# Kernel tuning notes

Measured on AMD Instinct MI355X. Metric: run time of the kernel, lower is better.

## Reference

```python
import jax, jax.numpy as jnp
import numpy as np

B, L = 16, 4096
D_IN, D_OUT, D_MODEL, N_LAYERS, N_STATE = 257, 257, 256, 4, 32  # 32 complex modes (= d_state 64 real)


def setup_inputs() -> dict:
    key = jax.random.key(0)
    ks = iter(jax.random.split(key, 24))
    nrm = lambda shape, s=0.02: jax.random.normal(next(ks), shape, jnp.float32) * s
    H, N = D_MODEL, N_STATE
    return {
        "x": jax.random.normal(next(ks), (B, L, D_IN, 2), jnp.float32),
        "enc_Wr": nrm((D_MODEL, D_IN)), "enc_Wi": nrm((D_MODEL, D_IN)),
        "enc_br": jnp.zeros((D_MODEL,), jnp.float32), "enc_bi": jnp.zeros((D_MODEL,), jnp.float32),
        # per layer (N_LAYERS) and per complex branch (2: real-branch S4D, imag-branch S4D)
        "s4_log_dt": jax.random.uniform(next(ks), (N_LAYERS, 2, H), jnp.float32,
                                        minval=float(np.log(0.001)), maxval=float(np.log(0.1))),
        "s4_log_A_real": jnp.broadcast_to(jnp.log(0.5 * jnp.ones((H, N), jnp.float32)), (N_LAYERS, 2, H, N)) + 0.0,
        "s4_A_imag": jnp.broadcast_to(jnp.pi * jnp.arange(N, dtype=jnp.float32), (N_LAYERS, 2, H, N)) + 0.0,
        "s4_C": jax.random.normal(next(ks), (N_LAYERS, 2, H, N, 2), jnp.float32) * (0.5 ** 0.5),
        "s4_D": jax.random.normal(next(ks), (N_LAYERS, 2, H), jnp.float32),
        "s4_Wout": nrm((N_LAYERS, 2, 2 * H, H)), "s4_bout": jnp.zeros((N_LAYERS, 2, 2 * H), jnp.float32),
        "ln_gamma": jnp.ones((N_LAYERS, 2, H), jnp.float32), "ln_beta": jnp.zeros((N_LAYERS, 2, H), jnp.float32),
        "dec_Wr": nrm((D_OUT, D_MODEL)), "dec_Wi": nrm((D_OUT, D_MODEL)),
        "dec_br": jnp.zeros((D_OUT,), jnp.float32), "dec_bi": jnp.zeros((D_OUT,), jnp.float32),
    }


def complex_linear(xr, xi, Wr, Wi, br, bi):
    yr = xr @ Wr.T - xi @ Wi.T + br
    yi = xr @ Wi.T + xi @ Wr.T + bi
    return yr, yi


def s4d_branch(u, log_dt, log_A_real, A_imag, C2, D, Wout, bout):
    """Standard S4D-minimal layer. u: (B, H, L) real."""
    Ln = u.shape[-1]
    dt = jnp.exp(log_dt)                            # (H,)
    A = -jnp.exp(log_A_real) + 1j * A_imag          # (H, N) complex
    C = C2[..., 0] + 1j * C2[..., 1]                # (H, N)
    dtA = A * dt[:, None]                           # (H, N)
    Cmod = C * (jnp.exp(dtA) - 1.0) / A
    vand = jnp.exp(dtA[..., None] * jnp.arange(Ln)) # (H, N, L)
    k = 2.0 * jnp.einsum('hn,hnl->hl', Cmod, vand).real  # (H, L)
    kf = jnp.fft.rfft(k, n=2 * Ln)
    uf = jnp.fft.rfft(u, n=2 * Ln)
    y = jnp.fft.irfft(uf * kf[None], n=2 * Ln)[..., :Ln]  # causal conv
    y = y + u * D[:, None]
    y = jax.nn.gelu(y, approximate=False)
    y = jnp.einsum('oh,bhl->bol', Wout, y) + bout[None, :, None]  # 1x1 conv to 2H
    a, g = jnp.split(y, 2, axis=1)                  # GLU over channel dim
    return a * jax.nn.sigmoid(g)


def layer_norm(x, gamma, beta):
    # x: (B, L, H), normalize over H (biased variance, like torch LayerNorm)
    mu = x.mean(-1, keepdims=True)
    var = x.var(-1, keepdims=True)
    return (x - mu) / jnp.sqrt(var + 1e-5) * gamma + beta


def reference(x, enc_Wr, enc_Wi, enc_br, enc_bi,
              s4_log_dt, s4_log_A_real, s4_A_imag, s4_C, s4_D, s4_Wout, s4_bout,
              ln_gamma, ln_beta, dec_Wr, dec_Wi, dec_br, dec_bi):
    xr, xi = complex_linear(x[..., 0], x[..., 1], enc_Wr, enc_Wi, enc_br, enc_bi)  # (B, L, H)
    xr = xr.swapaxes(-1, -2)  # (B, H, L)
    xi = xi.swapaxes(-1, -2)
    for l in range(N_LAYERS):
        sr = lambda u: s4d_branch(u, s4_log_dt[l, 0], s4_log_A_real[l, 0], s4_A_imag[l, 0],
                                  s4_C[l, 0], s4_D[l, 0], s4_Wout[l, 0], s4_bout[l, 0])
        si = lambda u: s4d_branch(u, s4_log_dt[l, 1], s4_log_A_real[l, 1], s4_A_imag[l, 1],
                                  s4_C[l, 1], s4_D[l, 1], s4_Wout[l, 1], s4_bout[l, 1])
        zr = sr(xr) - si(xi)
        zi = sr(xi) + si(xr)
        xr = xr + zr  # residual (dropout = identity)
        xi = xi + zi
        # post-norm over d_model (separate LN for real/imag parts)
        xr = layer_norm(xr.swapaxes(-1, -2), ln_gamma[l, 0], ln_beta[l, 0]).swapaxes(-1, -2)
        xi = layer_norm(xi.swapaxes(-1, -2), ln_gamma[l, 1], ln_beta[l, 1]).swapaxes(-1, -2)
    xr = xr.swapaxes(-1, -2)  # (B, L, H)
    xi = xi.swapaxes(-1, -2)
    yr, yi = complex_linear(xr, xi, dec_Wr, dec_Wi, dec_br, dec_bi)  # (B, L, D_OUT)
    return jnp.stack([yr, yi], axis=-1)
```

## Files before the change

### kernel.cpp

```cpp
#include <hip/hip_runtime.h>

typedef unsigned short ushort_t;
typedef unsigned int uint_t;
typedef __attribute__((ext_vector_type(8))) short short8;
typedef __attribute__((ext_vector_type(4))) float f32x4;

#define B_    16
#define L_    4096
#define H_    256
#define N_    32
#define DIN_  257
#define DOUT_ 257
#define NL_   4
#define Q_    128
#define NC_   32
#define BL_   (B_*L_)
#define NH_   (N_*H_)
#define PLANE_ 16777216
#define SSZ_  4194304
#define EPK_  520

__device__ __forceinline__ float bfu(ushort_t u) {
    union { uint_t i; float f; } v; v.i = ((uint_t)u) << 16; return v.f;
}
__device__ __forceinline__ ushort_t f2bf(float f) {
    union { float f; uint_t i; } v; v.f = f;
    uint_t x = v.i;
    return (ushort_t)((x + 0x7FFFu + ((x >> 16) & 1u)) >> 16);
}
__device__ __forceinline__ uint2 pack4(float a, float b, float c, float d) {
    uint2 r;
    r.x = (uint_t)f2bf(a) | ((uint_t)f2bf(b) << 16);
    r.y = (uint_t)f2bf(c) | ((uint_t)f2bf(d) << 16);
    return r;
}
__device__ __forceinline__ float ldi(const void* p, size_t i, int f32) {
    return f32 ? ((const float*)p)[i] : bfu(((const ushort_t*)p)[i]);
}

__device__ __forceinline__ void gl16(const ushort_t* g, ushort_t* l) {
    __builtin_amdgcn_global_load_lds(
        (const __attribute__((address_space(1))) uint_t*)g,
        (__attribute__((address_space(3))) uint_t*)l, 16, 0, 0);
}

__device__ __forceinline__ uint4 ld8bf(const void* W, size_t eoff, int f32) {
    uint4 r;
    if (f32) {
        const float* p = (const float*)W + eoff;
        float4 a = *(const float4*)p;
        float4 b = *(const float4*)(p + 4);
        r.x = (uint_t)f2bf(a.x) | ((uint_t)f2bf(a.y) << 16);
        r.y = (uint_t)f2bf(a.z) | ((uint_t)f2bf(a.w) << 16);
        r.z = (uint_t)f2bf(b.x) | ((uint_t)f2bf(b.y) << 16);
        r.w = (uint_t)f2bf(b.z) | ((uint_t)f2bf(b.w) << 16);
    } else {
        r = *(const uint4*)((const ushort_t*)W + eoff);
    }
    return r;
}

__device__ __forceinline__ uint4 ld8r(const void* x, size_t eoff, int f32) {
    uint4 r;
    if (f32) {
        const float* p = (const float*)x + eoff;
        float2 a = *(const float2*)p;
        float2 b = *(const float2*)(p + 2);
        float2 c = *(const float2*)(p + 4);
        float2 d = *(const float2*)(p + 6);
        r.x = (uint_t)f2bf(a.x) | ((uint_t)f2bf(a.y) << 16);
        r.y = (uint_t)f2bf(b.x) | ((uint_t)f2bf(b.y) << 16);
        r.z = (uint_t)f2bf(c.x) | ((uint_t)f2bf(c.y) << 16);
        r.w = (uint_t)f2bf(d.x) | ((uint_t)f2bf(d.y) << 16);
    } else {
        const uint_t* q = (const uint_t*)((const ushort_t*)x + eoff);
        r.x = q[0]; r.y = q[1]; r.z = q[2]; r.w = q[3];
    }
    return r;
}

__device__ __forceinline__ short8 negbf(short8 v) {
    short8 r;
#pragma unroll
    for (int i = 0; i < 8; ++i) r[i] = (short)(v[i] ^ (short)0x8000);
    return r;
}

#define MFMA16(a, b, c) __builtin_amdgcn_mfma_f32_16x16x32_bf16((a), (b), (c), 0, 0, 0)

__global__ void probe_kernel(const void* __restrict__ x, int* __restrict__ flag) {
    __shared__ int cnt;
    if (threadIdx.x == 0) cnt = 0;
    __syncthreads();
    uint_t w = ((const uint_t*)x)[threadIdx.x];
    float f = bfu((ushort_t)(w & 0xFFFF));
    float a = fabsf(f);
    if (a > 1e-5f && a < 100.f) atomicAdd(&cnt, 1);
    __syncthreads();
    if (threadIdx.x == 0) *flag = (cnt > 128) ? 0 : 1;
}

__global__ __launch_bounds__(256) void param_kernel(
        const void* __restrict__ log_dt, const void* __restrict__ lAr,
        const void* __restrict__ Aim, const void* __restrict__ C2,
        float* __restrict__ params, const int* __restrict__ dfl) {
    int f32 = *dfl;
    int idx = blockIdx.x * 256 + threadIdx.x;
    int h  = idx & (H_ - 1);
    int n  = (idx >> 8) & (N_ - 1);
    int lb = idx >> 13;
    float dt = expf(ldi(log_dt, lb * H_ + h, f32));
    size_t pin = (size_t)(lb * H_ + h) * N_ + n;
    float Ar = -expf(ldi(lAr, pin, f32));
    float Ai = ldi(Aim, pin, f32);
    float Cr = ldi(C2, pin * 2, f32), Ci = ldi(C2, pin * 2 + 1, f32);
    float dr = Ar * dt, di = Ai * dt;
    float e  = expf(dr);
    float wr = e * cosf(di), wi = e * sinf(di);
    float Er = wr - 1.0f, Ei = wi;
    float inv = 1.0f / (Ar * Ar + Ai * Ai);
    float Fr = (Er * Ar + Ei * Ai) * inv;
    float Fi = (Ei * Ar - Er * Ai) * inv;
    float ctr = 2.0f * (Cr * Fr - Ci * Fi);
    float cti = 2.0f * (Cr * Fi + Ci * Fr);
    float eq = expf((float)Q_ * dr);
    float ph = (float)Q_ * di;
    float wqr = eq * cosf(ph), wqi = eq * sinf(ph);
    float* pb = params + (size_t)lb * 6 * NH_;
    int o = n * H_ + h;
    pb[0 * NH_ + o] = wr;  pb[1 * NH_ + o] = wi;
    pb[2 * NH_ + o] = ctr; pb[3 * NH_ + o] = cti;
    pb[4 * NH_ + o] = wqr; pb[5 * NH_ + o] = wqi;
}

__global__ __launch_bounds__(256) void pack_enc(
        const void* __restrict__ Wr, const void* __restrict__ Wi,
        ushort_t* __restrict__ Wp, const int* __restrict__ dfl) {
    int f32 = *dfl;
    int n = blockIdx.x;
    for (int k = threadIdx.x; k < 260; k += 256) {
        float wr = 0.f, wi = 0.f;
        if (k < DIN_) {
            wr = ldi(Wr, (size_t)n * DIN_ + k, f32);
            wi = ldi(Wi, (size_t)n * DIN_ + k, f32);
        }
        Wp[(size_t)n * EPK_ + 2 * k]             = f2bf(wr);
        Wp[(size_t)n * EPK_ + 2 * k + 1]         = f2bf(-wi);
        Wp[(size_t)(256 + n) * EPK_ + 2 * k]     = f2bf(wi);
        Wp[(size_t)(256 + n) * EPK_ + 2 * k + 1] = f2bf(wr);
    }
}

__global__ __launch_bounds__(256) void enc_gemm(
        const void* __restrict__ x, const ushort_t* __restrict__ Wp,
        const void* __restrict__ br, const void* __restrict__ bi,
        ushort_t* __restrict__ xr, ushort_t* __restrict__ xi,
        const int* __restrict__ dfl) {
    __shared__ __align__(16) ushort_t As[8192];
    __shared__ __align__(16) ushort_t Brs[4096];
    __shared__ __align__(16) ushort_t Bis[4096];
    int f32 = *dfl;
    int m0 = blockIdx.x * 128, n0 = blockIdx.y * 64;
    int tid = threadIdx.x;
    int w = tid >> 6, l = tid & 63;
    int rb = w * 32;
    int lr = l & 15, lk = (l >> 4) << 4, lsw = (l & 7) << 4;
    int arow = tid >> 1;
    int ahalf = (tid & 1) << 6;
    int asw = (arow & 7) << 4;
    int brow = tid >> 2;
    int bq = (tid & 3) << 5;
    int bsw = (brow & 7) << 4;
    f32x4 z4 = {0.f, 0.f, 0.f, 0.f};
    f32x4 aR[2][4], aI[2][4];
#pragma unroll
    for (int mi = 0; mi < 2; ++mi)
#pragma unroll
        for (int nj = 0; nj < 4; ++nj) { aR[mi][nj] = z4; aI[mi][nj] = z4; }

    for (int k0 = 0; k0 < 512; k0 += 64) {
        if (k0) __syncthreads();
        {
            char* pa = (char*)As + arow * 128;
            size_t xbase = (size_t)(m0 + arow) * 2 * DIN_ + k0;
#pragma unroll
            for (int cc = 0; cc < 4; ++cc) {
                int cb = ahalf + cc * 16;
                uint4 v = ld8r(x, xbase + (cb >> 1), f32);
                *(uint4*)(pa + (cb ^ asw)) = v;
            }
        }
        {
            const ushort_t* wr_p = Wp + (size_t)(n0 + brow) * EPK_ + k0;
            const ushort_t* wi_p = Wp + (size_t)(256 + n0 + brow) * EPK_ + k0;
            char* pr_ = (char*)Brs + brow * 128;
            char* pi_ = (char*)Bis + brow * 128;
#pragma unroll
            for (int cc = 0; cc < 2; ++cc) {
                int cb = bq + cc * 16;
                *(uint4*)(pr_ + (cb ^ bsw)) = *(const uint4*)(wr_p + (cb >> 1));
                *(uint4*)(pi_ + (cb ^ bsw)) = *(const uint4*)(wi_p + (cb >> 1));
            }
        }
        __syncthreads();
#pragma unroll
        for (int ks = 0; ks < 2; ++ks) {
            int off = (ks * 64 + lk) ^ lsw;
            short8 a0 = *(const short8*)((const char*)As + (rb + lr) * 128 + off);
            short8 a1 = *(const short8*)((const char*)As + (rb + 16 + lr) * 128 + off);
#pragma unroll
            for (int nj = 0; nj < 4; ++nj) {
                short8 wr_ = *(const short8*)((const char*)Brs + (nj * 16 + lr) * 128 + off);
                short8 wi_ = *(const short8*)((const char*)Bis + (nj * 16 + lr) * 128 + off);
                aR[0][nj] = MFMA16(a0, wr_, aR[0][nj]);
                aR[1][nj] = MFMA16(a1, wr_, aR[1][nj]);
                aI[0][nj] = MFMA16(a0, wi_, aI[0][nj]);
                aI[1][nj] = MFMA16(a1, wi_, aI[1][nj]);
            }
        }
    }
    float xre8[8], xim8[8];
#pragma unroll
    for (int mi = 0; mi < 2; ++mi)
#pragma unroll
        for (int r = 0; r < 4; ++r) {
            int row = m0 + rb + mi * 16 + ((l >> 4) << 2) + r;
            size_t pi = (size_t)row * DIN_ + 256;
            float re, im;
            if (f32) { float2 v = ((const float2*)x)[pi]; re = v.x; im = v.y; }
            else { uint_t v = ((const uint_t*)x)[pi];
                   re = bfu((ushort_t)(v & 0xFFFF)); im = bfu((ushort_t)(v >> 16)); }
            xre8[mi * 4 + r] = re; xim8[mi * 4 + r] = im;
        }
#pragma unroll
    for (int nj = 0; nj < 4; ++nj) {
        int col = n0 + nj * 16 + lr;
        float wRr = bfu(Wp[(size_t)col * EPK_ + 512]);
        float wRi = bfu(Wp[(size_t)col * EPK_ + 513]);
        float wIr = bfu(Wp[(size_t)(256 + col) * EPK_ + 512]);
        float wIi = bfu(Wp[(size_t)(256 + col) * EPK_ + 513]);
        float bR = ldi(br, col, f32), bI = ldi(bi, col, f32);
#pragma unroll
        for (int mi = 0; mi < 2; ++mi)
#pragma unroll
            for (int r = 0; r < 4; ++r) {
                int row = m0 + rb + mi * 16 + ((l >> 4) << 2) + r;
                int q = mi * 4 + r;
                float re = aR[mi][nj][r] + xre8[q] * wRr + xim8[q] * wRi + bR;
                float im = aI[mi][nj][r] + xre8[q] * wIr + xim8[q] * wIi + bI;
                size_t off = (size_t)row * H_ + col;
                xr[off] = f2bf(re);
                xi[off] = f2bf(im);
            }
    }
}

__global__ __launch_bounds__(256) void pass_a(
        const ushort_t* __restrict__ U, const float* __restrict__ P, ushort_t* __restrict__ S) {
    int c = blockIdx.x, b = blockIdx.y, h = threadIdx.x;
    float wr[N_], wi[N_], sr[N_], si[N_];
#pragma unroll
    for (int n = 0; n < N_; ++n) {
        wr[n] = P[n * H_ + h]; wi[n] = P[NH_ + n * H_ + h];
        sr[n] = 0.f; si[n] = 0.f;
    }
    const ushort_t* u = U + (size_t)(b * L_ + c * Q_) * H_ + h;
    float uvn = bfu(u[0]);
    for (int t = 0; t < Q_; ++t) {
        float uv = uvn;
        int tn = (t + 1 < Q_) ? t + 1 : t;
        uvn = bfu(u[(size_t)tn * H_]);
#pragma unroll
        for (int n = 0; n < N_; ++n) {
            float nr = fmaf(wr[n], sr[n], fmaf(-wi[n], si[n], uv));
            si[n] = fmaf(wr[n], si[n], wi[n] * sr[n]);
            sr[n] = nr;
        }
    }
    size_t o = (size_t)(b * NC_ + c) * N_ * H_ + h;
#pragma unroll
    for (int n = 0; n < N_; ++n) {
        S[o + n * H_] = f2bf(sr[n]);
        S[o + n * H_ + SSZ_] = f2bf(si[n]);
    }
}

__global__ __launch_bounds__(256) void pass_b(
        const float* __restrict__ P, ushort_t* __restrict__ S) {
    int n = blockIdx.x, b = blockIdx.y, h = threadIdx.x;
    float wqr = P[4 * NH_ + n * H_ + h], wqi = P[5 * NH_ + n * H_ + h];
    float Xr = 0.f, Xi = 0.f;
    for (int c = 0; c < NC_; ++c) {
        size_t idx = ((size_t)(b * NC_ + c) * N_ + n) * H_ + h;
        float lr = bfu(S[idx]), li = bfu(S[idx + SSZ_]);
        S[idx] = f2bf(Xr); S[idx + SSZ_] = f2bf(Xi);
        float nr = fmaf(wqr, Xr, fmaf(-wqi, Xi, lr));
        Xi = fmaf(wqr, Xi, fmaf(wqi, Xr, li));
        Xr = nr;
    }
}

__global__ __launch_bounds__(256) void pass_c(
        const ushort_t* __restrict__ U, const float* __restrict__ P,
        const ushort_t* __restrict__ S, const void* __restrict__ Dp, int doff,
        ushort_t* __restrict__ G, const int* __restrict__ dfl) {
    int f32 = *dfl;
    int c = blockIdx.x, b = blockIdx.y;
    int tid = threadIdx.x;
    int h = blockIdx.z * 128 + (tid >> 1);
    int nb = (tid & 1) * 16;
    float wr[16], wi[16], cr[16], ci[16], sr[16], si[16];
#pragma unroll
    for (int i = 0; i < 16; ++i) {
        int o = (nb + i) * H_ + h;
        wr[i] = P[o]; wi[i] = P[NH_ + o];
        cr[i] = P[2 * NH_ + o]; ci[i] = P[3 * NH_ + o];
    }
    size_t so = (size_t)(b * NC_ + c) * N_ * H_ + h;
#pragma unroll
    for (int i = 0; i < 16; ++i) {
        sr[i] = bfu(S[so + (nb + i) * H_]);
        si[i] = bfu(S[so + (nb + i) * H_ + SSZ_]);
    }
    float Dv = ldi(Dp, (size_t)doff + h, f32);
    const ushort_t* u = U + (size_t)(b * L_ + c * Q_) * H_ + h;
    ushort_t* g = G + (size_t)(b * L_ + c * Q_) * H_ + h;
    float uvn = bfu(u[0]);
    for (int t = 0; t < Q_; ++t) {
        float uv = uvn;
        int tn = (t + 1 < Q_) ? t + 1 : t;
        uvn = bfu(u[(size_t)tn * H_]);
        float a0 = 0.f, a1 = 0.f;
#pragma unroll
        for (int i = 0; i < 16; ++i) {
            float nr = fmaf(wr[i], sr[i], fmaf(-wi[i], si[i], uv));
            si[i] = fmaf(wr[i], si[i], wi[i] * sr[i]);
            sr[i] = nr;
            if (i & 1) a1 = fmaf(cr[i], sr[i], fmaf(-ci[i], si[i], a1));
            else       a0 = fmaf(cr[i], sr[i], fmaf(-ci[i], si[i], a0));
        }
        float acc = a0 + a1;
        acc += __shfl_xor(acc, 1, 64);
        float y = fmaf(Dv, uv, acc);
        float ge = 0.5f * y * (1.0f + erff(y * 0.70710678118654752f));
        if ((tid & 1) == 0) g[(size_t)t * H_] = f2bf(ge);
    }
}

__global__ __launch_bounds__(256) void wout_gemm(
        const ushort_t* __restrict__ Gb, const void* __restrict__ W, size_t woff,
        const void* __restrict__ bo, int boff, ushort_t* __restrict__ Z, int mode,
        const int* __restrict__ dfl) {
    __shared__ __align__(16) ushort_t As[8192];
    __shared__ __align__(16) ushort_t Bs[8192];
    int f32 = *dfl;
    int m0 = blockIdx.x * 128, n0 = blockIdx.y * 64;
    int tid = threadIdx.x;
    int w = tid >> 6, l = tid & 63;
    int rb = w * 32;
    int lr = l & 15, lk = (l >> 4) << 4;
    int lsw = (l & 7) << 4;
    int arow = tid >> 3;
    int acb  = ((tid & 7) << 4) ^ ((arow & 7) << 4);
    int brow = tid >> 1;
    int bhalf = (tid & 1) << 6;
    int bsw = (brow & 7) << 4;
    int wrow = (brow < 64) ? (n0 + brow) : (192 + n0 + brow);
    f32x4 z4 = {0.f, 0.f, 0.f, 0.f};
    f32x4 acc[2][8];
#pragma unroll
    for (int mi = 0; mi < 2; ++mi)
#pragma unroll
        for (int nj = 0; nj < 8; ++nj) acc[mi][nj] = z4;

    for (int k0 = 0; k0 < H_; k0 += 64) {
        if (k0) __syncthreads();
        {
            const ushort_t* src = Gb + (size_t)(m0 + arow) * H_ + k0 + (acb >> 1);
            ushort_t* dst = As + tid * 8;
#pragma unroll
            for (int ch = 0; ch < 4; ++ch)
                gl16(src + (size_t)ch * 32 * H_, dst + ch * 2048);
        }
        {
            size_t wb = woff + (size_t)wrow * H_ + k0;
            char* bp = (char*)Bs + brow * 128;
#pragma unroll
            for (int cc = 0; cc < 4; ++cc) {
                int cb = bhalf + cc * 16;
                uint4 v = ld8bf(W, wb + (cb >> 1), f32);
                *(uint4*)(bp + (cb ^ bsw)) = v;
            }
        }
        __syncthreads();
#pragma unroll
        for (int ks = 0; ks < 2; ++ks) {
            int off = (ks * 64 + lk) ^ lsw;
            short8 a0 = *(const short8*)((const char*)As + (rb + lr) * 128 + off);
            short8 a1 = *(const short8*)((const char*)As + (rb + 16 + lr) * 128 + off);
#pragma unroll
            for (int nj = 0; nj < 8; ++nj) {
                short8 bv = *(const short8*)((const char*)Bs + (nj * 16 + lr) * 128 + off);
                acc[0][nj] = MFMA16(a0, bv, acc[0][nj]);
                acc[1][nj] = MFMA16(a1, bv, acc[1][nj]);
            }
        }
    }
    float ba[4], bg[4];
#pragma unroll
    for (int nj = 0; nj < 4; ++nj) {
        ba[nj] = ldi(bo, (size_t)boff + n0 + nj * 16 + lr, f32);
        bg[nj] = ldi(bo, (size_t)boff + 256 + n0 + nj * 16 + lr, f32);
    }
#pragma unroll
    for (int mi = 0; mi < 2; ++mi)
#pragma unroll
        for (int nj = 0; nj < 4; ++nj)
#pragma unroll
            for (int r = 0; r < 4; ++r) {
                float av = acc[mi][nj][r] + ba[nj];
                float gv = acc[mi][nj + 4][r] + bg[nj];
                float s = av * (1.0f / (1.0f + expf(-gv)));
                int row = m0 + rb + mi * 16 + ((l >> 4) << 2) + r;
                size_t zo = (size_t)row * H_ + n0 + nj * 16 + lr;
                if (mode == 0)      Z[zo] = f2bf(s);
                else if (mode == 1) Z[zo] = f2bf(bfu(Z[zo]) + s);
                else                Z[zo] = f2bf(bfu(Z[zo]) - s);
            }
}

__global__ __launch_bounds__(256) void combine_ln(
        ushort_t* __restrict__ xr, ushort_t* __restrict__ xi,
        const ushort_t* __restrict__ zr, const ushort_t* __restrict__ zi,
        const void* __restrict__ gamma, const void* __restrict__ beta, int layer,
        const int* __restrict__ dfl) {
    __shared__ float red[4][4];
    int f32 = *dfl;
    int l = blockIdx.x, b = blockIdx.y, h = threadIdx.x;
    size_t row = (size_t)(b * L_ + l) * H_ + h;
    float vr = bfu(xr[row]) + bfu(zr[row]);
    float vi = bfu(xi[row]) + bfu(zi[row]);
    float s0 = vr, s1 = vr * vr, s2 = vi, s3 = vi * vi;
#pragma unroll
    for (int off = 32; off >= 1; off >>= 1) {
        s0 += __shfl_xor(s0, off, 64); s1 += __shfl_xor(s1, off, 64);
        s2 += __shfl_xor(s2, off, 64); s3 += __shfl_xor(s3, off, 64);
    }
    int wv = h >> 6;
    if ((h & 63) == 0) { red[wv][0] = s0; red[wv][1] = s1; red[wv][2] = s2; red[wv][3] = s3; }
    __syncthreads();
    float S0 = red[0][0] + red[1][0] + red[2][0] + red[3][0];
    float S1 = red[0][1] + red[1][1] + red[2][1] + red[3][1];
    float S2 = red[0][2] + red[1][2] + red[2][2] + red[3][2];
    float S3 = red[0][3] + red[1][3] + red[2][3] + red[3][3];
    const float invH = 1.0f / 256.0f;
    float mur = S0 * invH, varr = S1 * invH - mur * mur;
    float mui = S2 * invH, vari = S3 * invH - mui * mui;
    float gr = ldi(gamma, (size_t)(layer * 2 + 0) * H_ + h, f32);
    float br_ = ldi(beta, (size_t)(layer * 2 + 0) * H_ + h, f32);
    float gi = ldi(gamma, (size_t)(layer * 2 + 1) * H_ + h, f32);
    float bi_ = ldi(beta, (size_t)(layer * 2 + 1) * H_ + h, f32);
    xr[row] = f2bf((vr - mur) * rsqrtf(varr + 1e-5f) * gr + br_);
    xi[row] = f2bf((vi - mui) * rsqrtf(vari + 1e-5f) * gi + bi_);
}

__global__ __launch_bounds__(256) void dec_gemm(
        const ushort_t* __restrict__ xr, const ushort_t* __restrict__ xi,
        const void* __restrict__ Wr, const void* __restrict__ Wi,
        const void* __restrict__ br, const void* __restrict__ bi,
        void* __restrict__ out, const int* __restrict__ dfl) {
    __shared__ __align__(16) ushort_t Ars[8192];
    __shared__ __align__(16) ushort_t Ais[8192];
    __shared__ __align__(16) ushort_t Brs[4096];
    __shared__ __align__(16) ushort_t Bis[4096];
    int f32 = *dfl;
    int m0 = blockIdx.x * 128, n0 = blockIdx.y * 64;
    int tid = threadIdx.x;
    int w = tid >> 6, l = tid & 63;
    int rb = w * 32;
    int lr = l & 15, lk = (l >> 4) << 4, lsw = (l & 7) << 4;
    int arow = tid >> 3;
    int acb  = ((tid & 7) << 4) ^ ((arow & 7) << 4);
    int brow = tid >> 2;
    int bq   = (tid & 3) << 5;
    int bsw  = (brow & 7) << 4;
    int wrow = n0 + brow;
    bool bvalid = wrow < DOUT_;
    uint4 zz; zz.x = zz.y = zz.z = zz.w = 0u;
    f32x4 z4 = {0.f, 0.f, 0.f, 0.f};
    f32x4 aR[2][4], aI[2][4];
#pragma unroll
    for (int mi = 0; mi < 2; ++mi)
#pragma unroll
        for (int nj = 0; nj < 4; ++nj) { aR[mi][nj] = z4; aI[mi][nj] = z4; }

    for (int k0 = 0; k0 < H_; k0 += 64) {
        if (k0) __syncthreads();
        {
            size_t so = (size_t)(m0 + arow) * H_ + k0 + (acb >> 1);
            ushort_t* dr = Ars + tid * 8;
            ushort_t* di = Ais + tid * 8;
#pragma unroll
            for (int ch = 0; ch < 4; ++ch) {
                gl16(xr + so + (size_t)ch * 32 * H_, dr + ch * 2048);
                gl16(xi + so + (size_t)ch * 32 * H_, di + ch * 2048);
            }
        }
        {
            size_t wb = (size_t)wrow * H_ + k0 + (bq >> 1);
            char* pr_ = (char*)Brs + brow * 128;
            char* pi_ = (char*)Bis + brow * 128;
#pragma unroll
            for (int cc = 0; cc < 2; ++cc) {
                int cb = bq + cc * 16;
                uint4 vr = zz, vi = zz;
                if (bvalid) {
                    vr = ld8bf(Wr, wb + cc * 8, f32);
                    vi = ld8bf(Wi, wb + cc * 8, f32);
                }
                *(uint4*)(pr_ + (cb ^ bsw)) = vr;
                *(uint4*)(pi_ + (cb ^ bsw)) = vi;
            }
        }
        __syncthreads();
#pragma unroll
        for (int ks = 0; ks < 2; ++ks) {
            int off = (ks * 64 + lk) ^ lsw;
            short8 x0 = *(const short8*)((const char*)Ars + (rb + lr) * 128 + off);
            short8 x1 = *(const short8*)((const char*)Ars + (rb + 16 + lr) * 128 + off);
            short8 y0 = *(const short8*)((const char*)Ais + (rb + lr) * 128 + off);
            short8 y1 = *(const short8*)((const char*)Ais + (rb + 16 + lr) * 128 + off);
#pragma unroll
            for (int nj = 0; nj < 4; ++nj) {
                short8 wr_ = *(const short8*)((const char*)Brs + (nj * 16 + lr) * 128 + off);
                short8 wi_ = *(const short8*)((const char*)Bis + (nj * 16 + lr) * 128 + off);
                short8 wn = negbf(wi_);
                aR[0][nj] = MFMA16(x0, wr_, aR[0][nj]);
                aR[0][nj] = MFMA16(y0, wn,  aR[0][nj]);
                aR[1][nj] = MFMA16(x1, wr_, aR[1][nj]);
                aR[1][nj] = MFMA16(y1, wn,  aR[1][nj]);
                aI[0][nj] = MFMA16(x0, wi_, aI[0][nj]);
                aI[0][nj] = MFMA16(y0, wr_, aI[0][nj]);
                aI[1][nj] = MFMA16(x1, wi_, aI[1][nj]);
                aI[1][nj] = MFMA16(y1, wr_, aI[1][nj]);
            }
        }
    }
#pragma unroll
    for (int nj = 0; nj < 4; ++nj) {
        int col = n0 + nj * 16 + lr;
        if (col < DOUT_) {
            float bR = ldi(br, col, f32), bI = ldi(bi, col, f32);
#pragma unroll
            for (int mi = 0; mi < 2; ++mi)
#pragma unroll
                for (int r = 0; r < 4; ++r) {
                    int row = m0 + rb + mi * 16 + ((l >> 4) << 2) + r;
                    size_t pi = (size_t)row * DOUT_ + col;
                    float re = aR[mi][nj][r] + bR;
                    float im = aI[mi][nj][r] + bI;
                    if (f32) {
                        ((float2*)out)[pi] = make_float2(re, im);
                    } else {
                        ((uint_t*)out)[pi] = (uint_t)f2bf(re) | ((uint_t)f2bf(im) << 16);
                    }
                }
        }
    }
}

extern "C" void kernel_launch(void* const* d_in, const int* in_sizes, int n_in,
                              void* d_out, int out_size, void* d_ws, size_t ws_size,
                              hipStream_t stream) {
    const void* x      = d_in[0];
    const void* enc_Wr = d_in[1];
    const void* enc_Wi = d_in[2];
    const void* enc_br = d_in[3];
    const void* enc_bi = d_in[4];
    const void* log_dt = d_in[5];
    const void* lAr    = d_in[6];
    const void* Aim    = d_in[7];
    const void* C2     = d_in[8];
    const void* Dp     = d_in[9];
    const void* Wout   = d_in[10];
    const void* bout   = d_in[11];
    const void* gamma  = d_in[12];
    const void* beta   = d_in[13];
    const void* dec_Wr = d_in[14];
    const void* dec_Wi = d_in[15];
    const void* dec_br = d_in[16];
    const void* dec_bi = d_in[17];

    ushort_t* xr = (ushort_t*)d_ws;
    ushort_t* xi = xr + (size_t)PLANE_;
    ushort_t* gb = xi + (size_t)PLANE_;
    ushort_t* st = gb + (size_t)PLANE_;
    int*      fl = (int*)(st + (size_t)2 * SSZ_);
    float*    pr = (float*)(fl + 64);
    ushort_t* zr = (ushort_t*)d_out;
    ushort_t* zi = zr + (size_t)PLANE_;
    ushort_t* Wp = st;

    probe_kernel<<<1, 256, 0, stream>>>(x, fl);
    param_kernel<<<256, 256, 0, stream>>>(log_dt, lAr, Aim, C2, pr, fl);
    pack_enc<<<256, 256, 0, stream>>>(enc_Wr, enc_Wi, Wp, fl);
    enc_gemm<<<dim3(BL_ / 128, H_ / 64), 256, 0, stream>>>(x, Wp, enc_br, enc_bi, xr, xi, fl);

    for (int l = 0; l < NL_; ++l) {
        struct App { int br; const ushort_t* U; ushort_t* Zt; int mode; };
        App apps[4] = {
            {0, xr, zr, 0},
            {1, xi, zr, 2},
            {0, xi, zi, 0},
            {1, xr, zi, 1},
        };
        for (int a = 0; a < 4; ++a) {
            const float* P = pr + (size_t)(l * 2 + apps[a].br) * 6 * NH_;
            pass_a<<<dim3(NC_, B_), 256, 0, stream>>>(apps[a].U, P, st);
            pass_b<<<dim3(N_, B_), 256, 0, stream>>>(P, st);
            pass_c<<<dim3(NC_, B_, 2), 256, 0, stream>>>(apps[a].U, P, st,
                    Dp, (l * 2 + apps[a].br) * H_, gb, fl);
            wout_gemm<<<dim3(BL_ / 128, H_ / 64), 256, 0, stream>>>(gb,
                    Wout, (size_t)(l * 2 + apps[a].br) * 512 * H_,
                    bout, (l * 2 + apps[a].br) * 512,
                    apps[a].Zt, apps[a].mode, fl);
        }
        combine_ln<<<dim3(L_, B_), 256, 0, stream>>>(xr, xi, zr, zi, gamma, beta, l, fl);
    }

    dec_gemm<<<dim3(BL_ / 128, (DOUT_ + 63) / 64), 256, 0, stream>>>(
            xr, xi, dec_Wr, dec_Wi, dec_br, dec_bi, d_out, fl);
}
```

Baseline: 4.674 ms.

## Split encoder input into bf16 planes and stage scan inputs in LDS

Adds a repack kernel that splits the interleaved complex input into separate bf16 real and imaginary planes. The encoder GEMM then loads tiles with global_load_lds and computes the complex product with four MFMAs and a negated weight, replacing the old interleaved K=512 packing. The pass_a and pass_c scan kernels now preload their chunk of U into shared memory asynchronously instead of issuing strided per-timestep global loads. The repack adds an extra pass over the input and uses the output buffer as scratch.

New measurement: 4.509 ms. 3.5% less time.

```diff
diff --git a/kernel.cpp b/kernel.cpp
--- a/kernel.cpp
+++ b/kernel.cpp
@@ -18,7 +18,6 @@
 #define NH_   (N_*H_)
 #define PLANE_ 16777216
 #define SSZ_  4194304
-#define EPK_  520
 
 __device__ __forceinline__ float bfu(ushort_t u) {
     union { uint_t i; float f; } v; v.i = ((uint_t)u) << 16; return v.f;
@@ -56,25 +55,6 @@
         r.w = (uint_t)f2bf(b.z) | ((uint_t)f2bf(b.w) << 16);
     } else {
         r = *(const uint4*)((const ushort_t*)W + eoff);
-    }
-    return r;
-}
-
-__device__ __forceinline__ uint4 ld8r(const void* x, size_t eoff, int f32) {
-    uint4 r;
-    if (f32) {
-        const float* p = (const float*)x + eoff;
-        float2 a = *(const float2*)p;
-        float2 b = *(const float2*)(p + 2);
-        float2 c = *(const float2*)(p + 4);
-        float2 d = *(const float2*)(p + 6);
-        r.x = (uint_t)f2bf(a.x) | ((uint_t)f2bf(a.y) << 16);
-        r.y = (uint_t)f2bf(b.x) | ((uint_t)f2bf(b.y) << 16);
-        r.z = (uint_t)f2bf(c.x) | ((uint_t)f2bf(c.y) << 16);
-        r.w = (uint_t)f2bf(d.x) | ((uint_t)f2bf(d.y) << 16);
-    } else {
-        const uint_t* q = (const uint_t*)((const ushort_t*)x + eoff);
-        r.x = q[0]; r.y = q[1]; r.z = q[2]; r.w = q[3];
     }
     return r;
 }
@@ -133,30 +113,49 @@
     pb[4 * NH_ + o] = wqr; pb[5 * NH_ + o] = wqi;
 }
 
-__global__ __launch_bounds__(256) void pack_enc(
+__global__ __launch_bounds__(256) void repack_x(
+        const void* __restrict__ x, ushort_t* __restrict__ xre,
+        ushort_t* __restrict__ xim, const int* __restrict__ dfl) {
+    int f32 = *dfl;
+    size_t i = ((size_t)blockIdx.x * 256 + threadIdx.x) * 4;
+    int row = (int)(i >> 8);
+    int k = (int)(i & 255);
+    size_t src = (size_t)row * DIN_ + k;
+    float re[4], im[4];
+#pragma unroll
+    for (int j = 0; j < 4; ++j) {
+        if (f32) {
+            float2 v = ((const float2*)x)[src + j];
+            re[j] = v.x; im[j] = v.y;
+        } else {
+            uint_t v = ((const uint_t*)x)[src + j];
+            re[j] = bfu((ushort_t)(v & 0xFFFF));
+            im[j] = bfu((ushort_t)(v >> 16));
+        }
+    }
+    *(uint2*)(xre + i) = pack4(re[0], re[1], re[2], re[3]);
+    *(uint2*)(xim + i) = pack4(im[0], im[1], im[2], im[3]);
+}
+
+__global__ __launch_bounds__(256) void pack_encw(
         const void* __restrict__ Wr, const void* __restrict__ Wi,
-        ushort_t* __restrict__ Wp, const int* __restrict__ dfl) {
-    int f32 = *dfl;
-    int n = blockIdx.x;
-    for (int k = threadIdx.x; k < 260; k += 256) {
-        float wr = 0.f, wi = 0.f;
-        if (k < DIN_) {
-            wr = ldi(Wr, (size_t)n * DIN_ + k, f32);
-            wi = ldi(Wi, (size_t)n * DIN_ + k, f32);
-        }
-        Wp[(size_t)n * EPK_ + 2 * k]             = f2bf(wr);
-        Wp[(size_t)n * EPK_ + 2 * k + 1]         = f2bf(-wi);
-        Wp[(size_t)(256 + n) * EPK_ + 2 * k]     = f2bf(wi);
-        Wp[(size_t)(256 + n) * EPK_ + 2 * k + 1] = f2bf(wr);
-    }
+        ushort_t* __restrict__ Wpr, ushort_t* __restrict__ Wpi,
+        const int* __restrict__ dfl) {
+    int f32 = *dfl;
+    int n = blockIdx.x, k = threadIdx.x;
+    Wpr[n * 256 + k] = f2bf(ldi(Wr, (size_t)n * DIN_ + k, f32));
+    Wpi[n * 256 + k] = f2bf(ldi(Wi, (size_t)n * DIN_ + k, f32));
 }
 
 __global__ __launch_bounds__(256) void enc_gemm(
-        const void* __restrict__ x, const ushort_t* __restrict__ Wp,
-        const void* __restrict__ br, const void* __restrict__ bi,
-        ushort_t* __restrict__ xr, ushort_t* __restrict__ xi,
-        const int* __restrict__ dfl) {
-    __shared__ __align__(16) ushort_t As[8192];
+        const ushort_t* __restrict__ xre, const ushort_t* __restrict__ xim,
+        const ushort_t* __restrict__ Wpr, const ushort_t* __restrict__ Wpi,
+        const void* __restrict__ x, const void* __restrict__ eWr,
+        const void* __restrict__ eWi, const void* __restrict__ br,
+        const void* __restrict__ bi, ushort_t* __restrict__ xr,
+        ushort_t* __restrict__ xi_, const int* __restrict__ dfl) {
+    __shared__ __align__(16) ushort_t Ars[8192];
+    __shared__ __align__(16) ushort_t Ais[8192];
     __shared__ __align__(16) ushort_t Brs[4096];
     __shared__ __align__(16) ushort_t Bis[4096];
     int f32 = *dfl;
@@ -165,12 +164,12 @@
     int w = tid >> 6, l = tid & 63;
     int rb = w * 32;
     int lr = l & 15, lk = (l >> 4) << 4, lsw = (l & 7) << 4;
-    int arow = tid >> 1;
-    int ahalf = (tid & 1) << 6;
-    int asw = (arow & 7) << 4;
+    int arow = tid >> 3;
+    int acb  = ((tid & 7) << 4) ^ ((arow & 7) << 4);
     int brow = tid >> 2;
-    int bq = (tid & 3) << 5;
-    int bsw = (brow & 7) << 4;
+    int bq   = (tid & 3) << 5;
+    int bsw  = (brow & 7) << 4;
+    int wrow = n0 + brow;
     f32x4 z4 = {0.f, 0.f, 0.f, 0.f};
     f32x4 aR[2][4], aI[2][4];
 #pragma unroll
@@ -178,48 +177,55 @@
 #pragma unroll
         for (int nj = 0; nj < 4; ++nj) { aR[mi][nj] = z4; aI[mi][nj] = z4; }
 
-    for (int k0 = 0; k0 < 512; k0 += 64) {
+    for (int k0 = 0; k0 < H_; k0 += 64) {
         if (k0) __syncthreads();
         {
-            char* pa = (char*)As + arow * 128;
-            size_t xbase = (size_t)(m0 + arow) * 2 * DIN_ + k0;
-#pragma unroll
-            for (int cc = 0; cc < 4; ++cc) {
-                int cb = ahalf + cc * 16;
-                uint4 v = ld8r(x, xbase + (cb >> 1), f32);
-                *(uint4*)(pa + (cb ^ asw)) = v;
+            size_t so = (size_t)(m0 + arow) * H_ + k0 + (acb >> 1);
+            ushort_t* dr = Ars + tid * 8;
+            ushort_t* di = Ais + tid * 8;
+#pragma unroll
+            for (int ch = 0; ch < 4; ++ch) {
+                gl16(xre + so + (size_t)ch * 32 * H_, dr + ch * 2048);
+                gl16(xim + so + (size_t)ch * 32 * H_, di + ch * 2048);
             }
         }
         {
-            const ushort_t* wr_p = Wp + (size_t)(n0 + brow) * EPK_ + k0;
-            const ushort_t* wi_p = Wp + (size_t)(256 + n0 + brow) * EPK_ + k0;
             char* pr_ = (char*)Brs + brow * 128;
             char* pi_ = (char*)Bis + brow * 128;
 #pragma unroll
             for (int cc = 0; cc < 2; ++cc) {
                 int cb = bq + cc * 16;
-                *(uint4*)(pr_ + (cb ^ bsw)) = *(const uint4*)(wr_p + (cb >> 1));
-                *(uint4*)(pi_ + (cb ^ bsw)) = *(const uint4*)(wi_p + (cb >> 1));
+                *(uint4*)(pr_ + (cb ^ bsw)) =
+                    *(const uint4*)(Wpr + (size_t)wrow * H_ + k0 + (cb >> 1));
+                *(uint4*)(pi_ + (cb ^ bsw)) =
+                    *(const uint4*)(Wpi + (size_t)wrow * H_ + k0 + (cb >> 1));
             }
         }
         __syncthreads();
 #pragma unroll
         for (int ks = 0; ks < 2; ++ks) {
             int off = (ks * 64 + lk) ^ lsw;
-            short8 a0 = *(const short8*)((const char*)As + (rb + lr) * 128 + off);
-            short8 a1 = *(const short8*)((const char*)As + (rb + 16 + lr) * 128 + off);
+            short8 x0 = *(const short8*)((const char*)Ars + (rb + lr) * 128 + off);
+            short8 x1 = *(const short8*)((const char*)Ars + (rb + 16 + lr) * 128 + off);
+            short8 y0 = *(const short8*)((const char*)Ais + (rb + lr) * 128 + off);
+            short8 y1 = *(const short8*)((const char*)Ais + (rb + 16 + lr) * 128 + off);
 #pragma unroll
             for (int nj = 0; nj < 4; ++nj) {
                 short8 wr_ = *(const short8*)((const char*)Brs + (nj * 16 + lr) * 128 + off);
                 short8 wi_ = *(const short8*)((const char*)Bis + (nj * 16 + lr) * 128 + off);
-                aR[0][nj] = MFMA16(a0, wr_, aR[0][nj]);
-                aR[1][nj] = MFMA16(a1, wr_, aR[1][nj]);
-                aI[0][nj] = MFMA16(a0, wi_, aI[0][nj]);
-                aI[1][nj] = MFMA16(a1, wi_, aI[1][nj]);
-            }
-        }
-    }
-    float xre8[8], xim8[8];
+                short8 wn = negbf(wi_);
+                aR[0][nj] = MFMA16(x0, wr_, aR[0][nj]);
+                aR[0][nj] = MFMA16(y0, wn,  aR[0][nj]);
+                aR[1][nj] = MFMA16(x1, wr_, aR[1][nj]);
+                aR[1][nj] = MFMA16(y1, wn,  aR[1][nj]);
+                aI[0][nj] = MFMA16(x0, wi_, aI[0][nj]);
+                aI[0][nj] = MFMA16(y0, wr_, aI[0][nj]);
+                aI[1][nj] = MFMA16(x1, wi_, aI[1][nj]);
+                aI[1][nj] = MFMA16(y1, wr_, aI[1][nj]);
+            }
+        }
+    }
+    float xcr[8], xci[8];
 #pragma unroll
     for (int mi = 0; mi < 2; ++mi)
 #pragma unroll
@@ -230,15 +236,13 @@
             if (f32) { float2 v = ((const float2*)x)[pi]; re = v.x; im = v.y; }
             else { uint_t v = ((const uint_t*)x)[pi];
                    re = bfu((ushort_t)(v & 0xFFFF)); im = bfu((ushort_t)(v >> 16)); }
-            xre8[mi * 4 + r] = re; xim8[mi * 4 + r] = im;
+            xcr[mi * 4 + r] = re; xci[mi * 4 + r] = im;
         }
 #pragma unroll
     for (int nj = 0; nj < 4; ++nj) {
         int col = n0 + nj * 16 + lr;
-        float wRr = bfu(Wp[(size_t)col * EPK_ + 512]);
-        float wRi = bfu(Wp[(size_t)col * EPK_ + 513]);
-        float wIr = bfu(Wp[(size_t)(256 + col) * EPK_ + 512]);
-        float wIi = bfu(Wp[(size_t)(256 + col) * EPK_ + 513]);
+        float wcr = ldi(eWr, (size_t)col * DIN_ + 256, f32);
+        float wci = ldi(eWi, (size_t)col * DIN_ + 256, f32);
         float bR = ldi(br, col, f32), bI = ldi(bi, col, f32);
 #pragma unroll
         for (int mi = 0; mi < 2; ++mi)
@@ -246,30 +250,35 @@
             for (int r = 0; r < 4; ++r) {
                 int row = m0 + rb + mi * 16 + ((l >> 4) << 2) + r;
                 int q = mi * 4 + r;
-                float re = aR[mi][nj][r] + xre8[q] * wRr + xim8[q] * wRi + bR;
-                float im = aI[mi][nj][r] + xre8[q] * wIr + xim8[q] * wIi + bI;
+                float re = aR[mi][nj][r] + xcr[q] * wcr - xci[q] * wci + bR;
+                float im = aI[mi][nj][r] + xcr[q] * wci + xci[q] * wcr + bI;
                 size_t off = (size_t)row * H_ + col;
-                xr[off] = f2bf(re);
-                xi[off] = f2bf(im);
+                xr[off]  = f2bf(re);
+                xi_[off] = f2bf(im);
             }
     }
 }
 
 __global__ __launch_bounds__(256) void pass_a(
         const ushort_t* __restrict__ U, const float* __restrict__ P, ushort_t* __restrict__ S) {
+    __shared__ __align__(16) ushort_t Us[Q_ * H_];
     int c = blockIdx.x, b = blockIdx.y, h = threadIdx.x;
+    const ushort_t* ub = U + (size_t)(b * L_ + c * Q_) * H_;
+#pragma unroll
+    for (int p = 0; p < 16; ++p)
+        gl16(ub + p * 2048 + h * 8, Us + p * 2048 + h * 8);
     float wr[N_], wi[N_], sr[N_], si[N_];
 #pragma unroll
     for (int n = 0; n < N_; ++n) {
         wr[n] = P[n * H_ + h]; wi[n] = P[NH_ + n * H_ + h];
         sr[n] = 0.f; si[n] = 0.f;
     }
-    const ushort_t* u = U + (size_t)(b * L_ + c * Q_) * H_ + h;
-    float uvn = bfu(u[0]);
+    __syncthreads();
+    float uvn = bfu(Us[h]);
     for (int t = 0; t < Q_; ++t) {
         float uv = uvn;
         int tn = (t + 1 < Q_) ? t + 1 : t;
-        uvn = bfu(u[(size_t)tn * H_]);
+        uvn = bfu(Us[tn * H_ + h]);
 #pragma unroll
         for (int n = 0; n < N_; ++n) {
             float nr = fmaf(wr[n], sr[n], fmaf(-wi[n], si[n], uv));
@@ -304,11 +313,21 @@
         const ushort_t* __restrict__ U, const float* __restrict__ P,
         const ushort_t* __restrict__ S, const void* __restrict__ Dp, int doff,
         ushort_t* __restrict__ G, const int* __restrict__ dfl) {
+    __shared__ __align__(16) ushort_t Us[Q_ * 128];
     int f32 = *dfl;
     int c = blockIdx.x, b = blockIdx.y;
     int tid = threadIdx.x;
-    int h = blockIdx.z * 128 + (tid >> 1);
+    int wv = tid >> 6, l = tid & 63;
+    int hl = tid >> 1;
+    int h = blockIdx.z * 128 + hl;
     int nb = (tid & 1) * 16;
+    const ushort_t* ub = U + (size_t)(b * L_ + c * Q_) * H_ + blockIdx.z * 128;
+#pragma unroll
+    for (int p = 0; p < 8; ++p) {
+        int row = p * 16 + wv * 4 + (l >> 4);
+        gl16(ub + (size_t)row * H_ + (l & 15) * 8,
+             Us + (p * 16 + wv * 4) * 128 + l * 8);
+    }
     float wr[16], wi[16], cr[16], ci[16], sr[16], si[16];
 #pragma unroll
     for (int i = 0; i < 16; ++i) {
@@ -323,13 +342,13 @@
         si[i] = bfu(S[so + (nb + i) * H_ + SSZ_]);
     }
     float Dv = ldi(Dp, (size_t)doff + h, f32);
-    const ushort_t* u = U + (size_t)(b * L_ + c * Q_) * H_ + h;
     ushort_t* g = G + (size_t)(b * L_ + c * Q_) * H_ + h;
-    float uvn = bfu(u[0]);
+    __syncthreads();
+    float uvn = bfu(Us[hl]);
     for (int t = 0; t < Q_; ++t) {
         float uv = uvn;
         int tn = (t + 1 < Q_) ? t + 1 : t;
-        uvn = bfu(u[(size_t)tn * H_]);
+        uvn = bfu(Us[tn * 128 + hl]);
         float a0 = 0.f, a1 = 0.f;
 #pragma unroll
         for (int i = 0; i < 16; ++i) {
@@ -599,12 +618,17 @@
     float*    pr = (float*)(fl + 64);
     ushort_t* zr = (ushort_t*)d_out;
     ushort_t* zi = zr + (size_t)PLANE_;
-    ushort_t* Wp = st;
+    ushort_t* xre = zr;
+    ushort_t* xim = zi;
+    ushort_t* Wpr = st;
+    ushort_t* Wpi = st + 65536;
 
     probe_kernel<<<1, 256, 0, stream>>>(x, fl);
     param_kernel<<<256, 256, 0, stream>>>(log_dt, lAr, Aim, C2, pr, fl);
-    pack_enc<<<256, 256, 0, stream>>>(enc_Wr, enc_Wi, Wp, fl);
-    enc_gemm<<<dim3(BL_ / 128, H_ / 64), 256, 0, stream>>>(x, Wp, enc_br, enc_bi, xr, xi, fl);
+    repack_x<<<16384, 256, 0, stream>>>(x, xre, xim, fl);
+    pack_encw<<<256, 256, 0, stream>>>(enc_Wr, enc_Wi, Wpr, Wpi, fl);
+    enc_gemm<<<dim3(BL_ / 128, H_ / 64), 256, 0, stream>>>(xre, xim, Wpr, Wpi,
+            x, enc_Wr, enc_Wi, enc_br, enc_bi, xr, xi, fl);
 
     for (int l = 0; l < NL_; ++l) {
         struct App { int br; const ushort_t* U; ushort_t* Zt; int mode; };
```
